# Optimization experiments

Hardware: AMD Instinct MI355X
Metric: run time of the kernel (lower is better)

## Reference

```python
import jax, jax.numpy as jnp
import numpy as np
import math

B, SQ, SK, D = 32, 2048, 2048, 64


def setup_inputs() -> dict:
    key = jax.random.key(0)
    kq, kk, kv, km = jax.random.split(key, 4)
    Q = jax.random.normal(kq, (B, SQ, D), dtype=jnp.float32)
    K = jax.random.normal(kk, (B, SK, D), dtype=jnp.float32)
    V = jax.random.normal(kv, (B, SK, D), dtype=jnp.float32)
    mask = jax.random.randint(km, (B, SQ, SK), 0, 2) > 0  # bool, True = keep
    return {"Q": Q, "K": K, "V": V, "mask": mask}


def reference(Q, K, V, mask):
    dim_qk = Q.shape[-1]
    # [B, Sq, Sk] = Q @ K^T / sqrt(d)
    attn_score = jnp.einsum("bqd,bkd->bqk", Q, K) / math.sqrt(dim_qk)
    attn_score = jnp.where(mask, attn_score, jnp.float32(-1e9))
    attn_score = jax.nn.softmax(attn_score, axis=-1)
    output = jnp.einsum("bqk,bkd->bqd", attn_score, V)
    return (attn_score, output)
```

## Files before the change

kernel.cpp:

```cpp
#include <hip/hip_runtime.h>
#include <math.h>

#define NB 32
#define SQL 2048
#define SKL 2048
#define DH 64
#define EPITCH (SKL + 8)

typedef __attribute__((ext_vector_type(8))) short short8;
typedef __attribute__((ext_vector_type(4))) float f32x4;

__device__ __forceinline__ unsigned short f2bf(float f) {
    unsigned int u = __float_as_uint(f);
    u += 0x7FFFu + ((u >> 16) & 1u);
    return (unsigned short)(u >> 16);
}
__device__ __forceinline__ float bf2f(unsigned short h) {
    return __uint_as_float(((unsigned int)h) << 16);
}
__device__ __forceinline__ short8 pack8(const float4& a, const float4& b) {
    short8 r;
    r[0] = (short)f2bf(a.x); r[1] = (short)f2bf(a.y);
    r[2] = (short)f2bf(a.z); r[3] = (short)f2bf(a.w);
    r[4] = (short)f2bf(b.x); r[5] = (short)f2bf(b.y);
    r[6] = (short)f2bf(b.z); r[7] = (short)f2bf(b.w);
    return r;
}

__global__ __launch_bounds__(512, 4)
void sdpa_mfma_kernel(const float* __restrict__ Qp, const float* __restrict__ Kp,
                      const float* __restrict__ Vp, const int* __restrict__ Mp,
                      float* __restrict__ Pout, float* __restrict__ Oout)
{
    __shared__ unsigned short e_sh[16 * EPITCH];
    __shared__ float l_part[8][16];
    __shared__ float inv_l[16];
    __shared__ f32x4 o_red[4 * 64];

    const int tid  = threadIdx.x;
    const int w    = tid >> 6;
    const int lane = tid & 63;
    const int quad = lane >> 4;
    const int s    = lane & 15;
    const int blk  = blockIdx.x;
    const int b    = blk >> 7;
    const int qt   = blk & 127;
    const int g0   = (b << 11) + (qt << 4);

    const float* qrow = Qp + (size_t)(g0 + s) * DH + quad * 8;
    const float4 q0 = *reinterpret_cast<const float4*>(qrow);
    const float4 q1 = *reinterpret_cast<const float4*>(qrow + 4);
    const float4 q2 = *reinterpret_cast<const float4*>(qrow + 32);
    const float4 q3 = *reinterpret_cast<const float4*>(qrow + 36);
    const short8 aq0 = pack8(q0, q1);
    const short8 aq1 = pack8(q2, q3);

    const size_t kvb = (size_t)b * SKL * DH;

    float l_acc[4] = {0.f, 0.f, 0.f, 0.f};
#pragma unroll 2
    for (int nt = 0; nt < 16; ++nt) {
        const int j0 = nt * 128 + w * 16;
        const float* kb = Kp + kvb + (size_t)(j0 + s) * DH + quad * 8;
        const float4 k0 = *reinterpret_cast<const float4*>(kb);
        const float4 k1 = *reinterpret_cast<const float4*>(kb + 4);
        const float4 k2 = *reinterpret_cast<const float4*>(kb + 32);
        const float4 k3 = *reinterpret_cast<const float4*>(kb + 36);
        const short8 bk0 = pack8(k0, k1);
        const short8 bk1 = pack8(k2, k3);

        f32x4 c = {0.f, 0.f, 0.f, 0.f};
        c = __builtin_amdgcn_mfma_f32_16x16x32_bf16(aq0, bk0, c, 0, 0, 0);
        c = __builtin_amdgcn_mfma_f32_16x16x32_bf16(aq1, bk1, c, 0, 0, 0);

        const int* mb = Mp + (size_t)(g0 + quad * 4) * SKL + j0 + s;
#pragma unroll
        for (int r = 0; r < 4; ++r) {
            const int   mk = mb[r * SKL];
            const float e  = mk ? exp2f(c[r] * 0.18033688011112042f) : 0.0f;
            l_acc[r] += e;
            e_sh[(quad * 4 + r) * EPITCH + j0 + s] = f2bf(e);
        }
    }

#pragma unroll
    for (int off = 1; off <= 8; off <<= 1) {
#pragma unroll
        for (int r = 0; r < 4; ++r)
            l_acc[r] += __shfl_xor(l_acc[r], off, 64);
    }
    if (s == 0) {
#pragma unroll
        for (int r = 0; r < 4; ++r)
            l_part[w][quad * 4 + r] = l_acc[r];
    }
    __syncthreads();
    if (tid < 16) {
        float t = 0.f;
#pragma unroll
        for (int wv = 0; wv < 8; ++wv) t += l_part[wv][tid];
        inv_l[tid] = 1.0f / t;
    }
    __syncthreads();

    float* pb = Pout + (size_t)g0 * SKL;
#pragma unroll 4
    for (int i = tid; i < 16 * (SKL / 4); i += 512) {
        const int row = i >> 9;
        const int c4  = (i & 511) << 2;
        const unsigned long long ev =
            *reinterpret_cast<const unsigned long long*>(&e_sh[row * EPITCH + c4]);
        const float il = inv_l[row];
        float4 pv;
        pv.x = bf2f((unsigned short)(ev))       * il;
        pv.y = bf2f((unsigned short)(ev >> 16)) * il;
        pv.z = bf2f((unsigned short)(ev >> 32)) * il;
        pv.w = bf2f((unsigned short)(ev >> 48)) * il;
        *reinterpret_cast<float4*>(pb + (size_t)row * SKL + c4) = pv;
    }

    f32x4 oacc = {0.f, 0.f, 0.f, 0.f};
    const int d0 = (w & 3) * 16;
    const int h  = w >> 2;
    const float* vb = Vp + kvb + d0 + s;
#pragma unroll 2
    for (int kt = h * 32; kt < h * 32 + 32; ++kt) {
        const int k0 = kt * 32 + quad * 8;
        const short8 ap =
            *reinterpret_cast<const short8*>(&e_sh[s * EPITCH + k0]);
        const float* vk = vb + (size_t)k0 * DH;
        short8 bv;
#pragma unroll
        for (int j = 0; j < 8; ++j)
            bv[j] = (short)f2bf(vk[(size_t)j * DH]);
        oacc = __builtin_amdgcn_mfma_f32_16x16x32_bf16(ap, bv, oacc, 0, 0, 0);
    }
    if (w >= 4)
        o_red[(w - 4) * 64 + lane] = oacc;
    __syncthreads();
    if (w < 4) {
        const f32x4 o2 = o_red[w * 64 + lane];
#pragma unroll
        for (int r = 0; r < 4; ++r) {
            const int m = quad * 4 + r;
            Oout[(size_t)(g0 + m) * DH + d0 + s] = (oacc[r] + o2[r]) * inv_l[m];
        }
    }
}

extern "C" void kernel_launch(void* const* d_in, const int* in_sizes, int n_in,
                              void* d_out, int out_size, void* d_ws, size_t ws_size,
                              hipStream_t stream) {
    const float* Q = (const float*)d_in[0];
    const float* K = (const float*)d_in[1];
    const float* V = (const float*)d_in[2];
    const int*   M = (const int*)d_in[3];

    float* Pout = (float*)d_out;
    float* Oout = Pout + (size_t)NB * SQL * SKL;

    const int blocks = NB * (SQL / 16);
    sdpa_mfma_kernel<<<blocks, 512, 0, stream>>>(Q, K, V, M, Pout, Oout);
}
```

Before: 1.179 ms.

## Precast Q/K to bf16 and pre-transpose V in prepass kernels

After: 1.070 ms. -9.2%, faster.

```diff
diff --git a/kernel.cpp b/kernel.cpp
--- a/kernel.cpp
+++ b/kernel.cpp
@@ -18,18 +18,54 @@
 __device__ __forceinline__ float bf2f(unsigned short h) {
     return __uint_as_float(((unsigned int)h) << 16);
 }
-__device__ __forceinline__ short8 pack8(const float4& a, const float4& b) {
-    short8 r;
-    r[0] = (short)f2bf(a.x); r[1] = (short)f2bf(a.y);
-    r[2] = (short)f2bf(a.z); r[3] = (short)f2bf(a.w);
-    r[4] = (short)f2bf(b.x); r[5] = (short)f2bf(b.y);
-    r[6] = (short)f2bf(b.z); r[7] = (short)f2bf(b.w);
-    return r;
+
+__global__ __launch_bounds__(256)
+void cvt_bf16_kernel(const float* __restrict__ in, unsigned short* __restrict__ out, int n4)
+{
+    const int i = blockIdx.x * 256 + threadIdx.x;
+    if (i < n4) {
+        const float4 v = reinterpret_cast<const float4*>(in)[i];
+        ushort4 o;
+        o.x = f2bf(v.x); o.y = f2bf(v.y); o.z = f2bf(v.z); o.w = f2bf(v.w);
+        reinterpret_cast<ushort4*>(out)[i] = o;
+    }
+}
+
+__global__ __launch_bounds__(256)
+void vtrans_kernel(const float* __restrict__ V, unsigned short* __restrict__ Vt)
+{
+    __shared__ float tile[64][65];
+    const int b  = blockIdx.x >> 5;
+    const int kt = blockIdx.x & 31;
+    const int t  = threadIdx.x;
+    const int c4 = (t & 15) << 2;
+    const int r0 = t >> 4;
+    const float* vb = V + ((size_t)b * SKL + (size_t)kt * 64) * DH;
+#pragma unroll
+    for (int i = 0; i < 4; ++i) {
+        const int r = r0 + i * 16;
+        const float4 v = *reinterpret_cast<const float4*>(vb + (size_t)r * DH + c4);
+        tile[r][c4] = v.x; tile[r][c4 + 1] = v.y; tile[r][c4 + 2] = v.z; tile[r][c4 + 3] = v.w;
+    }
+    __syncthreads();
+    unsigned short* ob = Vt + (size_t)b * DH * SKL + (size_t)kt * 64;
+#pragma unroll
+    for (int i = 0; i < 4; ++i) {
+        const int d = r0 + i * 16;
+        ushort4 o;
+        o.x = f2bf(tile[c4 + 0][d]);
+        o.y = f2bf(tile[c4 + 1][d]);
+        o.z = f2bf(tile[c4 + 2][d]);
+        o.w = f2bf(tile[c4 + 3][d]);
+        *reinterpret_cast<ushort4*>(ob + (size_t)d * SKL + c4) = o;
+    }
 }
 
 __global__ __launch_bounds__(512, 4)
-void sdpa_mfma_kernel(const float* __restrict__ Qp, const float* __restrict__ Kp,
-                      const float* __restrict__ Vp, const int* __restrict__ Mp,
+void sdpa_mfma_kernel(const unsigned short* __restrict__ Qb,
+                      const unsigned short* __restrict__ Kb,
+                      const unsigned short* __restrict__ Vtb,
+                      const int* __restrict__ Mp,
                       float* __restrict__ Pout, float* __restrict__ Oout)
 {
     __shared__ unsigned short e_sh[16 * EPITCH];
@@ -47,27 +83,19 @@
     const int qt   = blk & 127;
     const int g0   = (b << 11) + (qt << 4);
 
-    const float* qrow = Qp + (size_t)(g0 + s) * DH + quad * 8;
-    const float4 q0 = *reinterpret_cast<const float4*>(qrow);
-    const float4 q1 = *reinterpret_cast<const float4*>(qrow + 4);
-    const float4 q2 = *reinterpret_cast<const float4*>(qrow + 32);
-    const float4 q3 = *reinterpret_cast<const float4*>(qrow + 36);
-    const short8 aq0 = pack8(q0, q1);
-    const short8 aq1 = pack8(q2, q3);
+    const unsigned short* qrow = Qb + (size_t)(g0 + s) * DH + quad * 8;
+    const short8 aq0 = *reinterpret_cast<const short8*>(qrow);
+    const short8 aq1 = *reinterpret_cast<const short8*>(qrow + 32);
 
     const size_t kvb = (size_t)b * SKL * DH;
 
     float l_acc[4] = {0.f, 0.f, 0.f, 0.f};
-#pragma unroll 2
+#pragma unroll 4
     for (int nt = 0; nt < 16; ++nt) {
         const int j0 = nt * 128 + w * 16;
-        const float* kb = Kp + kvb + (size_t)(j0 + s) * DH + quad * 8;
-        const float4 k0 = *reinterpret_cast<const float4*>(kb);
-        const float4 k1 = *reinterpret_cast<const float4*>(kb + 4);
-        const float4 k2 = *reinterpret_cast<const float4*>(kb + 32);
-        const float4 k3 = *reinterpret_cast<const float4*>(kb + 36);
-        const short8 bk0 = pack8(k0, k1);
-        const short8 bk1 = pack8(k2, k3);
+        const unsigned short* kb = Kb + kvb + (size_t)(j0 + s) * DH + quad * 8;
+        const short8 bk0 = *reinterpret_cast<const short8*>(kb);
+        const short8 bk1 = *reinterpret_cast<const short8*>(kb + 32);
 
         f32x4 c = {0.f, 0.f, 0.f, 0.f};
         c = __builtin_amdgcn_mfma_f32_16x16x32_bf16(aq0, bk0, c, 0, 0, 0);
@@ -76,7 +104,7 @@
         const int* mb = Mp + (size_t)(g0 + quad * 4) * SKL + j0 + s;
 #pragma unroll
         for (int r = 0; r < 4; ++r) {
-            const int   mk = mb[r * SKL];
+            const int   mk = mb[(size_t)r * SKL];
             const float e  = mk ? exp2f(c[r] * 0.18033688011112042f) : 0.0f;
             l_acc[r] += e;
             e_sh[(quad * 4 + r) * EPITCH + j0 + s] = f2bf(e);
@@ -122,17 +150,13 @@
     f32x4 oacc = {0.f, 0.f, 0.f, 0.f};
     const int d0 = (w & 3) * 16;
     const int h  = w >> 2;
-    const float* vb = Vp + kvb + d0 + s;
-#pragma unroll 2
+    const unsigned short* vtr = Vtb + (size_t)b * DH * SKL + (size_t)(d0 + s) * SKL;
+#pragma unroll 4
     for (int kt = h * 32; kt < h * 32 + 32; ++kt) {
         const int k0 = kt * 32 + quad * 8;
         const short8 ap =
             *reinterpret_cast<const short8*>(&e_sh[s * EPITCH + k0]);
-        const float* vk = vb + (size_t)k0 * DH;
-        short8 bv;
-#pragma unroll
-        for (int j = 0; j < 8; ++j)
-            bv[j] = (short)f2bf(vk[(size_t)j * DH]);
+        const short8 bv = *reinterpret_cast<const short8*>(vtr + k0);
         oacc = __builtin_amdgcn_mfma_f32_16x16x32_bf16(ap, bv, oacc, 0, 0, 0);
     }
     if (w >= 4)
@@ -159,6 +183,15 @@
     float* Pout = (float*)d_out;
     float* Oout = Pout + (size_t)NB * SQL * SKL;
 
+    unsigned short* Qb = (unsigned short*)d_ws;
+    unsigned short* Kb = Qb + (size_t)NB * SQL * DH;
+    unsigned short* Vt = Kb + (size_t)NB * SKL * DH;
+
+    const int n4q = NB * SQL * DH / 4;
+    cvt_bf16_kernel<<<n4q / 256, 256, 0, stream>>>(Q, Qb, n4q);
+    cvt_bf16_kernel<<<n4q / 256, 256, 0, stream>>>(K, Kb, n4q);
+    vtrans_kernel<<<NB * 32, 256, 0, stream>>>(V, Vt);
+
     const int blocks = NB * (SQL / 16);
-    sdpa_mfma_kernel<<<blocks, 512, 0, stream>>>(Q, K, V, M, Pout, Oout);
+    sdpa_mfma_kernel<<<blocks, 512, 0, stream>>>(Qb, Kb, Vt, M, Pout, Oout);
 }
```
